# Kernel tuning notes

Measured on AMD Instinct MI355X. Metric: run time of the kernel, lower is better.

The kernel has to match this reference:

```python
import jax, jax.numpy as jnp
import numpy as np

N_NODES = 50000
BN_EPS = 1e-5


def graph_conv(x, row, col, ew, n):
    # deg from source indices only (matches torch.bincount(row))
    deg = jnp.zeros((n,), x.dtype).at[row].add(1.0)
    dinv = jnp.where(deg > 0, deg ** -0.5, 0.0)
    norm = dinv[row] * ew * dinv[col]                     # [E]
    msg = norm[:, None] * x[row]                          # [E, F]
    return jax.ops.segment_sum(msg, col, num_segments=n)  # out[dst] += w * x[src]


def batch_norm(x, gamma, beta):
    # training-mode BN over the node (batch) dim, biased variance
    mu = jnp.mean(x, axis=0)
    var = jnp.mean((x - mu) ** 2, axis=0)
    return (x - mu) / jnp.sqrt(var + BN_EPS) * gamma + beta


def setup_inputs() -> dict:
    key = jax.random.key(0)
    ks = jax.random.split(key, 12)
    node_features = jax.random.normal(ks[0], (N_NODES, 100), dtype=jnp.float32)
    edge_index = jax.random.randint(ks[1], (2, 800000), 0, N_NODES, dtype=jnp.int64)
    edge_weights = jax.random.uniform(ks[2], (800000,), dtype=jnp.float32)
    def lin(k, fi, fo):
        lim = 1.0 / np.sqrt(fi)
        k1, k2 = jax.random.split(k)
        W = jax.random.uniform(k1, (fi, fo), minval=-lim, maxval=lim, dtype=jnp.float32)
        b = jax.random.uniform(k2, (fo,), minval=-lim, maxval=lim, dtype=jnp.float32)
        return W, b
    W0, b0 = lin(ks[3], 100, 128)
    W1, b1 = lin(ks[4], 128, 128)
    W2, b2 = lin(ks[5], 128, 64)
    return {
        "node_features": node_features, "edge_index": edge_index, "edge_weights": edge_weights,
        "W0": W0, "b0": b0, "g0": jnp.ones((128,), jnp.float32), "be0": jnp.zeros((128,), jnp.float32),
        "W1": W1, "b1": b1, "g1": jnp.ones((128,), jnp.float32), "be1": jnp.zeros((128,), jnp.float32),
        "W2": W2, "b2": b2,
    }


def reference(node_features, edge_index, edge_weights,
              W0, b0, g0, be0, W1, b1, g1, be1, W2, b2):
    n = node_features.shape[0]
    row, col = edge_index[0], edge_index[1]
    x = node_features
    # layer 0
    x = graph_conv(x, row, col, edge_weights, n)
    x = jax.nn.relu(batch_norm(x @ W0 + b0, g0, be0))
    # layer 1
    x = graph_conv(x, row, col, edge_weights, n)
    x = jax.nn.relu(batch_norm(x @ W1 + b1, g1, be1))
    # final layer (no BN/relu)
    x = graph_conv(x, row, col, edge_weights, n)
    return x @ W2 + b2
```

## Files before the change

kernel.cpp:

```cpp
#include <hip/hip_runtime.h>
#include <cstdint>

#define F0 100
#define FH 128
#define FO 64
#define PD 4
#define BN_EPS 1e-5f

typedef unsigned short ushort_t;
typedef unsigned int uint_t;

static inline int ceil_div(long long a, long long b) { return (int)((a + b - 1) / b); }

__device__ __forceinline__ float bf_lo(uint_t w) { return __uint_as_float(w << 16); }
__device__ __forceinline__ float bf_hi(uint_t w) { return __uint_as_float(w & 0xffff0000u); }
__device__ __forceinline__ uint_t f2bf(float f) {
  uint_t u = __float_as_uint(f);
  return (u + 0x7fffu + ((u >> 16) & 1u)) >> 16;
}
__device__ __forceinline__ uint_t pack2(float a, float b) {
  return f2bf(a) | (f2bf(b) << 16);
}


template <int K, int F, int TM, int BK, bool BN_A, bool A_BF16, bool OUT_BF16>
__device__ __forceinline__ void gemm2_body(int bid, const void* __restrict__ A_,
                                           const float* __restrict__ W,
                                           const float* __restrict__ bias,
                                           const float* __restrict__ scA,
                                           const float* __restrict__ shA,
                                           void* __restrict__ out_, int n) {
  constexpr int NCG = F / 4;
  constexpr int NRG = 256 / NCG;
  constexpr int BR = NRG * TM;
  constexpr int F4 = F / 4;

  __shared__ float sW[BK][F];
  __shared__ float sA[BR][BK];

  const int tid = threadIdx.x;
  const int cg = tid % NCG;
  const int rg = tid / NCG;
  const int row0 = bid * BR;

  float4 acc[TM];
#pragma unroll
  for (int t = 0; t < TM; ++t) acc[t] = make_float4(0.f, 0.f, 0.f, 0.f);

  const float4* W4 = (const float4*)W;
  const float4 z4 = make_float4(0.f, 0.f, 0.f, 0.f);

  for (int k0 = 0; k0 < K; k0 += BK) {
    for (int i = tid; i < BK * F4; i += 256) {
      int kk = i / F4, f4 = i % F4;
      int gk = k0 + kk;
      ((float4*)&sW[kk][0])[f4] = (gk < K) ? W4[(size_t)gk * F4 + f4] : z4;
    }
    for (int i = tid; i < BR * (BK / 4); i += 256) {
      int r = i / (BK / 4), k4 = i % (BK / 4);
      int gr = row0 + r;
      int gk = k0 + k4 * 4;
      float4 av = z4;
      if (gr < n && gk + 3 < K) {
        if (A_BF16) {
          uint2 u = ((const uint2*)A_)[(size_t)gr * (K / 4) + (gk >> 2)];
          av.x = bf_lo(u.x); av.y = bf_hi(u.x);
          av.z = bf_lo(u.y); av.w = bf_hi(u.y);
        } else {
          av = ((const float4*)A_)[(size_t)gr * (K / 4) + (gk >> 2)];
        }
        if (BN_A) {
          float4 sc = ((const float4*)scA)[gk >> 2];
          float4 sh = ((const float4*)shA)[gk >> 2];
          av.x = fmaxf(fmaf(av.x, sc.x, sh.x), 0.f);
          av.y = fmaxf(fmaf(av.y, sc.y, sh.y), 0.f);
          av.z = fmaxf(fmaf(av.z, sc.z, sh.z), 0.f);
          av.w = fmaxf(fmaf(av.w, sc.w, sh.w), 0.f);
        }
      }
      ((float4*)&sA[r][0])[k4] = av;
    }
    __syncthreads();
#pragma unroll 4
    for (int kk = 0; kk < BK; ++kk) {
      float4 w = ((const float4*)&sW[kk][0])[cg];
#pragma unroll
      for (int t = 0; t < TM; ++t) {
        float a = sA[rg * TM + t][kk];
        acc[t].x = fmaf(a, w.x, acc[t].x);
        acc[t].y = fmaf(a, w.y, acc[t].y);
        acc[t].z = fmaf(a, w.z, acc[t].z);
        acc[t].w = fmaf(a, w.w, acc[t].w);
      }
    }
    __syncthreads();
  }

  float4 bb = bias ? ((const float4*)bias)[cg] : z4;
#pragma unroll
  for (int t = 0; t < TM; ++t) {
    int gr = row0 + rg * TM + t;
    if (gr < n) {
      float4 v = acc[t];
      v.x += bb.x; v.y += bb.y; v.z += bb.z; v.w += bb.w;
      if (OUT_BF16) {
        ((uint2*)out_)[(size_t)gr * F4 + cg] = make_uint2(pack2(v.x, v.y), pack2(v.z, v.w));
      } else {
        ((float4*)out_)[(size_t)gr * F4 + cg] = v;
      }
    }
  }
}

template <int K, int F, int TM, int BK, bool BN_A, bool A_BF16, bool OUT_BF16>
__global__ __launch_bounds__(256) void gemm2_kernel(const void* __restrict__ A,
                                                    const float* __restrict__ W,
                                                    const float* __restrict__ bias,
                                                    const float* __restrict__ scA,
                                                    const float* __restrict__ shA,
                                                    void* __restrict__ out, int n) {
  gemm2_body<K, F, TM, BK, BN_A, A_BF16, OUT_BF16>(blockIdx.x, A, W, bias, scA, shA, out, n);
}


__global__ __launch_bounds__(256) void fused_gemm_hist_kernel(
    const float* __restrict__ A, const float* __restrict__ W, void* __restrict__ out, int n,
    int GB, const int* __restrict__ row, const int* __restrict__ col,
    int* __restrict__ degr_p, int* __restrict__ degc_p, int* __restrict__ posw, int E) {
  int bid = blockIdx.x;
  int r5 = bid % 5;
  int g = bid / 5;
  if (r5 == 0 && g < GB) {
    gemm2_body<F0, FH, 8, 16, false, false, true>(g, A, W, nullptr, nullptr, nullptr, out, n);
    return;
  }
  int h = (r5 == 0) ? (bid - GB) : (bid - (g + 1));
  int e = h * 256 + threadIdx.x;
  if (e >= E) return;
  atomicAdd(&degr_p[(size_t)row[e] * PD], 1);
  posw[e] = atomicAdd(&degc_p[(size_t)col[e] * PD], 1);
}


__global__ __launch_bounds__(256) void scan_fused_kernel(const int* __restrict__ degr_p,
                                                         const int* __restrict__ degc_p,
                                                         float* __restrict__ dinv,
                                                         int* __restrict__ startp,
                                                         int* __restrict__ bsums, int n,
                                                         int* __restrict__ ctr) {
  __shared__ int s[256];
  const int tid = threadIdx.x;
  int i = blockIdx.x * 256 + tid;
  int dc = 0;
  if (i < n) {
    int dr = degr_p[(size_t)i * PD];
    dc = degc_p[(size_t)i * PD];
    dinv[i] = (dr > 0) ? rsqrtf((float)dr) : 0.0f;
  }
  s[tid] = dc;
  __syncthreads();
  for (int off = 1; off < 256; off <<= 1) {
    int t = 0;
    if (tid >= off) t = s[tid - off];
    __syncthreads();
    if (tid >= off) s[tid] += t;
    __syncthreads();
  }
  if (i < n) startp[i] = s[tid] - dc;
  if (tid == 255) bsums[blockIdx.x] = s[255];
  __threadfence();
  __syncthreads();
  __shared__ int lastFlag;
  if (tid == 0) lastFlag = (atomicAdd(ctr, 1) == (int)gridDim.x - 1) ? 1 : 0;
  __syncthreads();
  if (!lastFlag) return;
  int nb = (int)gridDim.x;
  int v = (tid < nb) ? atomicAdd(&bsums[tid], 0) : 0;
  s[tid] = v;
  __syncthreads();
  for (int off = 1; off < 256; off <<= 1) {
    int t = 0;
    if (tid >= off) t = s[tid - off];
    __syncthreads();
    if (tid >= off) s[tid] += t;
    __syncthreads();
  }
  if (tid < nb) bsums[tid] = s[tid] - v;
}


__global__ __launch_bounds__(256) void csr_scatter2_kernel(const int* __restrict__ row,
                                                           const int* __restrict__ col,
                                                           const float* __restrict__ ew,
                                                           const float* __restrict__ dinv,
                                                           const int* __restrict__ startp,
                                                           const int* __restrict__ bsums,
                                                           const int* __restrict__ posw,
                                                           int2* __restrict__ ep, int E) {
  int e = blockIdx.x * blockDim.x + threadIdx.x;
  if (e >= E) return;
  int r = row[e], c = col[e];
  int pos = startp[c] + bsums[c >> 8] + posw[e];
  float coef = dinv[r] * ew[e] * dinv[c];
  ep[pos] = make_int2(r, __float_as_int(coef));
}


template <int F, bool DO_BN, bool OUT_F32>
__global__ __launch_bounds__(256) void conv_kernel(const ushort_t* __restrict__ x,
                                                   const int* __restrict__ startp,
                                                   const int* __restrict__ bsums,
                                                   const int* __restrict__ degc_p,
                                                   const int2* __restrict__ ep,
                                                   const float* __restrict__ bias,
                                                   const float* __restrict__ scale,
                                                   const float* __restrict__ shift,
                                                   void* __restrict__ out, int n) {
  constexpr int G2 = F / 8;
  constexpr int TPD = G2 / 2;
  long long tid = (long long)blockIdx.x * 256 + threadIdx.x;
  if (tid >= (long long)n * TPD) return;
  int dst = (int)(tid / TPD);
  int q = (int)(tid % TPD);
  int s0 = startp[dst] + bsums[dst >> 8];
  int d = degc_p[(size_t)dst * PD];
  const uint4* x4 = (const uint4*)x;

  float sc[16], sh[16];
  if (DO_BN) {
#pragma unroll
    for (int ch = 0; ch < 2; ++ch) {
      int g = q + ch * TPD;
#pragma unroll
      for (int j = 0; j < 8; ++j) {
        sc[ch * 8 + j] = scale[g * 8 + j];
        sh[ch * 8 + j] = shift[g * 8 + j];
      }
    }
  }

  float acc[16];
#pragma unroll
  for (int j = 0; j < 16; ++j) acc[j] = 0.f;

  for (int k = 0; k < d; ++k) {
    int2 e = ep[s0 + k];
    float c = __int_as_float(e.y);
    const uint4* xp = x4 + (size_t)e.x * G2 + q;
    uint4 v0 = xp[0];
    uint4 v1 = xp[TPD];
    uint_t vv[8] = {v0.x, v0.y, v0.z, v0.w, v1.x, v1.y, v1.z, v1.w};
#pragma unroll
    for (int hh = 0; hh < 8; ++hh) {
      float f0 = bf_lo(vv[hh]);
      float f1 = bf_hi(vv[hh]);
      if (DO_BN) {
        f0 = fmaxf(fmaf(f0, sc[2 * hh], sh[2 * hh]), 0.f);
        f1 = fmaxf(fmaf(f1, sc[2 * hh + 1], sh[2 * hh + 1]), 0.f);
      }
      acc[2 * hh] = fmaf(c, f0, acc[2 * hh]);
      acc[2 * hh + 1] = fmaf(c, f1, acc[2 * hh + 1]);
    }
  }

  if (bias) {
#pragma unroll
    for (int ch = 0; ch < 2; ++ch) {
      int g = q + ch * TPD;
#pragma unroll
      for (int j = 0; j < 8; ++j) acc[ch * 8 + j] += bias[g * 8 + j];
    }
  }

  if (OUT_F32) {
    float4* o4 = (float4*)out;
    size_t base = (size_t)dst * (F / 4);
    o4[base + 2 * q] = make_float4(acc[0], acc[1], acc[2], acc[3]);
    o4[base + 2 * q + 1] = make_float4(acc[4], acc[5], acc[6], acc[7]);
    o4[base + 2 * (q + TPD)] = make_float4(acc[8], acc[9], acc[10], acc[11]);
    o4[base + 2 * (q + TPD) + 1] = make_float4(acc[12], acc[13], acc[14], acc[15]);
  } else {
    uint4* o4 = (uint4*)out;
    size_t base = (size_t)dst * G2;
    o4[base + q] = make_uint4(pack2(acc[0], acc[1]), pack2(acc[2], acc[3]),
                              pack2(acc[4], acc[5]), pack2(acc[6], acc[7]));
    o4[base + q + TPD] = make_uint4(pack2(acc[8], acc[9]), pack2(acc[10], acc[11]),
                                    pack2(acc[12], acc[13]), pack2(acc[14], acc[15]));
  }
}


__global__ __launch_bounds__(256) void bn_stats_fast_kernel(const ushort_t* __restrict__ z,
                                                            float* __restrict__ sum,
                                                            float* __restrict__ sumsq,
                                                            const float* __restrict__ g,
                                                            const float* __restrict__ be,
                                                            float* __restrict__ scale,
                                                            float* __restrict__ shift,
                                                            int n, int* __restrict__ ctr) {
  const int tid = threadIdx.x;
  const int q = tid & 15;
  const int rg = tid >> 4;
  const uint4* z4 = (const uint4*)z;

  float s[8], s2[8];
#pragma unroll
  for (int j = 0; j < 8; ++j) { s[j] = 0.f; s2[j] = 0.f; }

  for (int r = blockIdx.x * 16 + rg; r < n; r += (int)gridDim.x * 16) {
    uint4 v = z4[(size_t)r * (FH / 8) + q];
    uint_t vv[4] = {v.x, v.y, v.z, v.w};
#pragma unroll
    for (int h = 0; h < 4; ++h) {
      float f0 = bf_lo(vv[h]);
      float f1 = bf_hi(vv[h]);
      s[2 * h] += f0;      s2[2 * h] += f0 * f0;
      s[2 * h + 1] += f1;  s2[2 * h + 1] += f1 * f1;
    }
  }

  __shared__ float red[256][8];
#pragma unroll
  for (int j = 0; j < 8; ++j) red[tid][j] = s[j];
  __syncthreads();
  for (int off = 128; off >= 16; off >>= 1) {
    if (tid < off) {
#pragma unroll
      for (int j = 0; j < 8; ++j) red[tid][j] += red[tid + off][j];
    }
    __syncthreads();
  }
  if (tid < 16) {
#pragma unroll
    for (int j = 0; j < 8; ++j) unsafeAtomicAdd(&sum[8 * tid + j], red[tid][j]);
  }
  __syncthreads();
#pragma unroll
  for (int j = 0; j < 8; ++j) red[tid][j] = s2[j];
  __syncthreads();
  for (int off = 128; off >= 16; off >>= 1) {
    if (tid < off) {
#pragma unroll
      for (int j = 0; j < 8; ++j) red[tid][j] += red[tid + off][j];
    }
    __syncthreads();
  }
  if (tid < 16) {
#pragma unroll
    for (int j = 0; j < 8; ++j) unsafeAtomicAdd(&sumsq[8 * tid + j], red[tid][j]);
  }
  __threadfence();
  __syncthreads();
  __shared__ int lastFlag;
  if (tid == 0) lastFlag = (atomicAdd(ctr, 1) == (int)gridDim.x - 1) ? 1 : 0;
  __syncthreads();
  if (lastFlag && tid < FH) {
    float S = atomicAdd(&sum[tid], 0.0f);
    float S2 = atomicAdd(&sumsq[tid], 0.0f);
    float invN = 1.0f / (float)n;
    float mean = S * invN;
    float var = fmaxf(S2 * invN - mean * mean, 0.0f);
    float sc = g[tid] / sqrtf(var + BN_EPS);
    scale[tid] = sc;
    shift[tid] = be[tid] - mean * sc;
  }
}


extern "C" void kernel_launch(void* const* d_in, const int* in_sizes, int n_in,
                              void* d_out, int out_size, void* d_ws, size_t ws_size,
                              hipStream_t stream) {
  const float* x   = (const float*)d_in[0];
  const int*   ei  = (const int*)d_in[1];
  const float* ew  = (const float*)d_in[2];
  const float* W0  = (const float*)d_in[3];
  const float* b0  = (const float*)d_in[4];
  const float* g0  = (const float*)d_in[5];
  const float* be0 = (const float*)d_in[6];
  const float* W1  = (const float*)d_in[7];
  const float* b1  = (const float*)d_in[8];
  const float* g1  = (const float*)d_in[9];
  const float* be1 = (const float*)d_in[10];
  const float* W2  = (const float*)d_in[11];
  const float* b2  = (const float*)d_in[12];

  const int n = in_sizes[0] / F0;
  const int E = in_sizes[2];
  const int* row = ei;
  const int* col = ei + E;

  ushort_t* bufA  = (ushort_t*)d_ws;
  ushort_t* bufB  = bufA + (size_t)n * FH;
  int2*   ep      = (int2*)(bufB + (size_t)n * FH);
  int*    degc_p  = (int*)(ep + E);
  int*    degr_p  = degc_p + (size_t)n * PD;
  float*  sum0    = (float*)(degr_p + (size_t)n * PD);
  float*  sumsq0  = sum0 + FH;
  float*  sum1    = sumsq0 + FH;
  float*  sumsq1  = sum1 + FH;
  int*    ctr     = (int*)(sumsq1 + FH);
  const size_t zero_bytes = (2 * (size_t)n * PD + 4 * FH + 3) * 4;
  int*    startp  = ctr + 3;
  float*  dinv    = (float*)(startp + n);
  int*    bsums   = (int*)(dinv + n);
  float*  scale0  = (float*)(bsums + 256);
  float*  shift0  = scale0 + FH;
  float*  scale1  = shift0 + FH;
  float*  shift1  = scale1 + FH;
  int*    posw    = (int*)bufB;

  const int nb = ceil_div(n, 256);
  const int GB = ceil_div(n, 64);
  const int HB = ceil_div(E, 256);
  const int CB_H = ceil_div((long long)n * (FH / 16), 256);
  const int CB_O = ceil_div((long long)n * (FO / 16), 256);

  (void)hipMemsetAsync(degc_p, 0, zero_bytes, stream);
  fused_gemm_hist_kernel<<<GB + HB, 256, 0, stream>>>(x, W0, bufA, n, GB, row, col,
                                                      degr_p, degc_p, posw, E);
  scan_fused_kernel<<<nb, 256, 0, stream>>>(degr_p, degc_p, dinv, startp, bsums, n, ctr + 0);
  csr_scatter2_kernel<<<HB, 256, 0, stream>>>(row, col, ew, dinv, startp, bsums, posw, ep, E);
  conv_kernel<FH, false, false><<<CB_H, 256, 0, stream>>>(
      bufA, startp, bsums, degc_p, ep, b0, nullptr, nullptr, bufB, n);
  bn_stats_fast_kernel<<<128, 256, 0, stream>>>(bufB, sum0, sumsq0, g0, be0, scale0, shift0,
                                                n, ctr + 1);
  conv_kernel<FH, true, false><<<CB_H, 256, 0, stream>>>(
      bufB, startp, bsums, degc_p, ep, nullptr, scale0, shift0, bufA, n);
  gemm2_kernel<FH, FH, 8, 32, false, true, true><<<GB, 256, 0, stream>>>(
      bufA, W1, b1, nullptr, nullptr, bufB, n);
  bn_stats_fast_kernel<<<128, 256, 0, stream>>>(bufB, sum1, sumsq1, g1, be1, scale1, shift1,
                                                n, ctr + 2);
  gemm2_kernel<FH, FO, 4, 32, true, true, true><<<GB, 256, 0, stream>>>(
      bufB, W2, nullptr, scale1, shift1, bufA, n);
  conv_kernel<FO, false, true><<<CB_O, 256, 0, stream>>>(
      bufA, startp, bsums, degc_p, ep, b2, nullptr, nullptr, (float*)d_out, n);
}
```

Measured before the change: 367.4 us.

## Fuse BatchNorm statistics into conv0 and gemm1 epilogues, drop separate stats passes

Removes the two standalone BN statistics kernels. The per-feature sum and sum-of-squares are now accumulated in the epilogues of the first aggregation kernel and the W1 GEMM kernel, each followed by an in-block reduction, global atomics and a last-block finalize of scale and shift. This avoids re-reading the 50000x128 bf16 intermediates twice and saves two launches. In exchange, every block now issues atomics and runs an extra shared-memory reduction. Statistics are also taken from the fp32 values before bf16 rounding, which slightly changes the numerics.

```diff
diff --git a/kernel.cpp b/kernel.cpp
--- a/kernel.cpp
+++ b/kernel.cpp
@@ -206,6 +206,134 @@
 }
 
 
+template <bool DO_BN>
+__device__ __forceinline__ void conv_accum_128(const ushort_t* __restrict__ x, int s0, int d,
+                                               int q, const int2* __restrict__ ep,
+                                               const float* __restrict__ sc,
+                                               const float* __restrict__ sh,
+                                               float* __restrict__ acc) {
+  constexpr int G2 = FH / 8;
+  constexpr int TPD = 8;
+  const uint4* x4 = (const uint4*)x;
+#pragma unroll
+  for (int j = 0; j < 16; ++j) acc[j] = 0.f;
+  for (int k = 0; k < d; ++k) {
+    int2 e = ep[s0 + k];
+    float c = __int_as_float(e.y);
+    const uint4* xp = x4 + (size_t)e.x * G2 + q;
+    uint4 v0 = xp[0];
+    uint4 v1 = xp[TPD];
+    uint_t vv[8] = {v0.x, v0.y, v0.z, v0.w, v1.x, v1.y, v1.z, v1.w};
+#pragma unroll
+    for (int hh = 0; hh < 8; ++hh) {
+      float f0 = bf_lo(vv[hh]);
+      float f1 = bf_hi(vv[hh]);
+      if (DO_BN) {
+        f0 = fmaxf(fmaf(f0, sc[2 * hh], sh[2 * hh]), 0.f);
+        f1 = fmaxf(fmaf(f1, sc[2 * hh + 1], sh[2 * hh + 1]), 0.f);
+      }
+      acc[2 * hh] = fmaf(c, f0, acc[2 * hh]);
+      acc[2 * hh + 1] = fmaf(c, f1, acc[2 * hh + 1]);
+    }
+  }
+}
+
+
+__global__ __launch_bounds__(256) void conv0_stats_kernel(
+    const ushort_t* __restrict__ x, const int* __restrict__ startp,
+    const int* __restrict__ bsums, const int* __restrict__ degc_p,
+    const int2* __restrict__ ep, const float* __restrict__ bias,
+    ushort_t* __restrict__ out, int n, const float* __restrict__ g,
+    const float* __restrict__ be, float* __restrict__ sum, float* __restrict__ sumsq,
+    float* __restrict__ scale, float* __restrict__ shift, int* __restrict__ ctr) {
+  const int tid = threadIdx.x;
+  const int dl = tid / 8;
+  const int q = tid % 8;
+
+  float s[16], s2[16];
+#pragma unroll
+  for (int j = 0; j < 16; ++j) { s[j] = 0.f; s2[j] = 0.f; }
+
+  for (int c = 0; c < 2; ++c) {
+    int dst = blockIdx.x * 64 + c * 32 + dl;
+    if (dst >= n) continue;
+    int s0 = startp[dst] + bsums[dst >> 8];
+    int d = degc_p[(size_t)dst * PD];
+    float acc[16];
+    conv_accum_128<false>(x, s0, d, q, ep, nullptr, nullptr, acc);
+#pragma unroll
+    for (int ch = 0; ch < 2; ++ch) {
+#pragma unroll
+      for (int j = 0; j < 8; ++j) {
+        int f = ch * 64 + 8 * q + j;
+        float v = acc[ch * 8 + j] + bias[f];
+        acc[ch * 8 + j] = v;
+        s[ch * 8 + j] += v;
+        s2[ch * 8 + j] += v * v;
+      }
+    }
+    uint4* o4 = (uint4*)out;
+    size_t base = (size_t)dst * (FH / 8);
+    o4[base + q] = make_uint4(pack2(acc[0], acc[1]), pack2(acc[2], acc[3]),
+                              pack2(acc[4], acc[5]), pack2(acc[6], acc[7]));
+    o4[base + q + 8] = make_uint4(pack2(acc[8], acc[9]), pack2(acc[10], acc[11]),
+                                  pack2(acc[12], acc[13]), pack2(acc[14], acc[15]));
+  }
+
+  __shared__ float red[32][8][16];
+#pragma unroll
+  for (int j = 0; j < 16; ++j) red[dl][q][j] = s[j];
+  __syncthreads();
+  for (int off = 16; off >= 1; off >>= 1) {
+    if (dl < off) {
+#pragma unroll
+      for (int j = 0; j < 16; ++j) red[dl][q][j] += red[dl + off][q][j];
+    }
+    __syncthreads();
+  }
+  if (dl == 0) {
+#pragma unroll
+    for (int j = 0; j < 16; ++j) {
+      int f = (j < 8) ? (8 * q + j) : (64 + 8 * q + (j - 8));
+      unsafeAtomicAdd(&sum[f], red[0][q][j]);
+    }
+  }
+  __syncthreads();
+#pragma unroll
+  for (int j = 0; j < 16; ++j) red[dl][q][j] = s2[j];
+  __syncthreads();
+  for (int off = 16; off >= 1; off >>= 1) {
+    if (dl < off) {
+#pragma unroll
+      for (int j = 0; j < 16; ++j) red[dl][q][j] += red[dl + off][q][j];
+    }
+    __syncthreads();
+  }
+  if (dl == 0) {
+#pragma unroll
+    for (int j = 0; j < 16; ++j) {
+      int f = (j < 8) ? (8 * q + j) : (64 + 8 * q + (j - 8));
+      unsafeAtomicAdd(&sumsq[f], red[0][q][j]);
+    }
+  }
+  __threadfence();
+  __syncthreads();
+  __shared__ int lastFlag;
+  if (tid == 0) lastFlag = (atomicAdd(ctr, 1) == (int)gridDim.x - 1) ? 1 : 0;
+  __syncthreads();
+  if (lastFlag && tid < FH) {
+    float S = atomicAdd(&sum[tid], 0.0f);
+    float S2 = atomicAdd(&sumsq[tid], 0.0f);
+    float invN = 1.0f / (float)n;
+    float mean = S * invN;
+    float var = fmaxf(S2 * invN - mean * mean, 0.0f);
+    float sc = g[tid] / sqrtf(var + BN_EPS);
+    scale[tid] = sc;
+    shift[tid] = be[tid] - mean * sc;
+  }
+}
+
+
 template <int F, bool DO_BN, bool OUT_F32>
 __global__ __launch_bounds__(256) void conv_kernel(const ushort_t* __restrict__ x,
                                                    const int* __restrict__ startp,
@@ -290,64 +418,107 @@
 }
 
 
-__global__ __launch_bounds__(256) void bn_stats_fast_kernel(const ushort_t* __restrict__ z,
-                                                            float* __restrict__ sum,
-                                                            float* __restrict__ sumsq,
-                                                            const float* __restrict__ g,
-                                                            const float* __restrict__ be,
-                                                            float* __restrict__ scale,
-                                                            float* __restrict__ shift,
-                                                            int n, int* __restrict__ ctr) {
+__global__ __launch_bounds__(256) void gemm1_stats_kernel(
+    const ushort_t* __restrict__ A, const float* __restrict__ W,
+    const float* __restrict__ bias, ushort_t* __restrict__ out, int n,
+    const float* __restrict__ g, const float* __restrict__ be, float* __restrict__ sum,
+    float* __restrict__ sumsq, float* __restrict__ scale, float* __restrict__ shift,
+    int* __restrict__ ctr) {
+  constexpr int K = FH, F = FH, TM = 8, BK = 32;
+  constexpr int NCG = F / 4;
+  constexpr int NRG = 256 / NCG;
+  constexpr int BR = NRG * TM;
+  constexpr int F4 = F / 4;
+
+  __shared__ float sW[BK][F];
+  __shared__ float sA[BR][BK];
+  __shared__ float red[NRG][NCG][4];
+
   const int tid = threadIdx.x;
-  const int q = tid & 15;
-  const int rg = tid >> 4;
-  const uint4* z4 = (const uint4*)z;
-
-  float s[8], s2[8];
-#pragma unroll
-  for (int j = 0; j < 8; ++j) { s[j] = 0.f; s2[j] = 0.f; }
-
-  for (int r = blockIdx.x * 16 + rg; r < n; r += (int)gridDim.x * 16) {
-    uint4 v = z4[(size_t)r * (FH / 8) + q];
-    uint_t vv[4] = {v.x, v.y, v.z, v.w};
-#pragma unroll
-    for (int h = 0; h < 4; ++h) {
-      float f0 = bf_lo(vv[h]);
-      float f1 = bf_hi(vv[h]);
-      s[2 * h] += f0;      s2[2 * h] += f0 * f0;
-      s[2 * h + 1] += f1;  s2[2 * h + 1] += f1 * f1;
-    }
-  }
-
-  __shared__ float red[256][8];
-#pragma unroll
-  for (int j = 0; j < 8; ++j) red[tid][j] = s[j];
-  __syncthreads();
-  for (int off = 128; off >= 16; off >>= 1) {
-    if (tid < off) {
-#pragma unroll
-      for (int j = 0; j < 8; ++j) red[tid][j] += red[tid + off][j];
-    }
-    __syncthreads();
-  }
-  if (tid < 16) {
-#pragma unroll
-    for (int j = 0; j < 8; ++j) unsafeAtomicAdd(&sum[8 * tid + j], red[tid][j]);
-  }
-  __syncthreads();
-#pragma unroll
-  for (int j = 0; j < 8; ++j) red[tid][j] = s2[j];
-  __syncthreads();
-  for (int off = 128; off >= 16; off >>= 1) {
-    if (tid < off) {
-#pragma unroll
-      for (int j = 0; j < 8; ++j) red[tid][j] += red[tid + off][j];
-    }
-    __syncthreads();
-  }
-  if (tid < 16) {
-#pragma unroll
-    for (int j = 0; j < 8; ++j) unsafeAtomicAdd(&sumsq[8 * tid + j], red[tid][j]);
+  const int cg = tid % NCG;
+  const int rg = tid / NCG;
+  const int row0 = blockIdx.x * BR;
+
+  float4 acc[TM];
+#pragma unroll
+  for (int t = 0; t < TM; ++t) acc[t] = make_float4(0.f, 0.f, 0.f, 0.f);
+
+  const float4* W4 = (const float4*)W;
+  const float4 z4 = make_float4(0.f, 0.f, 0.f, 0.f);
+
+  for (int k0 = 0; k0 < K; k0 += BK) {
+    for (int i = tid; i < BK * F4; i += 256) {
+      int kk = i / F4, f4 = i % F4;
+      ((float4*)&sW[kk][0])[f4] = W4[(size_t)(k0 + kk) * F4 + f4];
+    }
+    for (int i = tid; i < BR * (BK / 4); i += 256) {
+      int r = i / (BK / 4), k4 = i % (BK / 4);
+      int gr = row0 + r;
+      int gk = k0 + k4 * 4;
+      float4 av = z4;
+      if (gr < n) {
+        uint2 u = ((const uint2*)A)[(size_t)gr * (K / 4) + (gk >> 2)];
+        av.x = bf_lo(u.x); av.y = bf_hi(u.x);
+        av.z = bf_lo(u.y); av.w = bf_hi(u.y);
+      }
+      ((float4*)&sA[r][0])[k4] = av;
+    }
+    __syncthreads();
+#pragma unroll 4
+    for (int kk = 0; kk < BK; ++kk) {
+      float4 w = ((const float4*)&sW[kk][0])[cg];
+#pragma unroll
+      for (int t = 0; t < TM; ++t) {
+        float a = sA[rg * TM + t][kk];
+        acc[t].x = fmaf(a, w.x, acc[t].x);
+        acc[t].y = fmaf(a, w.y, acc[t].y);
+        acc[t].z = fmaf(a, w.z, acc[t].z);
+        acc[t].w = fmaf(a, w.w, acc[t].w);
+      }
+    }
+    __syncthreads();
+  }
+
+  float4 bb = ((const float4*)bias)[cg];
+  float4 s = z4, s2 = z4;
+#pragma unroll
+  for (int t = 0; t < TM; ++t) {
+    int gr = row0 + rg * TM + t;
+    if (gr < n) {
+      float4 v = acc[t];
+      v.x += bb.x; v.y += bb.y; v.z += bb.z; v.w += bb.w;
+      ((uint2*)out)[(size_t)gr * F4 + cg] = make_uint2(pack2(v.x, v.y), pack2(v.z, v.w));
+      s.x += v.x; s.y += v.y; s.z += v.z; s.w += v.w;
+      s2.x += v.x * v.x; s2.y += v.y * v.y; s2.z += v.z * v.z; s2.w += v.w * v.w;
+    }
+  }
+
+  red[rg][cg][0] = s.x; red[rg][cg][1] = s.y; red[rg][cg][2] = s.z; red[rg][cg][3] = s.w;
+  __syncthreads();
+  for (int off = 4; off >= 1; off >>= 1) {
+    if (rg < off) {
+#pragma unroll
+      for (int j = 0; j < 4; ++j) red[rg][cg][j] += red[rg + off][cg][j];
+    }
+    __syncthreads();
+  }
+  if (rg == 0) {
+#pragma unroll
+    for (int j = 0; j < 4; ++j) unsafeAtomicAdd(&sum[cg * 4 + j], red[0][cg][j]);
+  }
+  __syncthreads();
+  red[rg][cg][0] = s2.x; red[rg][cg][1] = s2.y; red[rg][cg][2] = s2.z; red[rg][cg][3] = s2.w;
+  __syncthreads();
+  for (int off = 4; off >= 1; off >>= 1) {
+    if (rg < off) {
+#pragma unroll
+      for (int j = 0; j < 4; ++j) red[rg][cg][j] += red[rg + off][cg][j];
+    }
+    __syncthreads();
+  }
+  if (rg == 0) {
+#pragma unroll
+    for (int j = 0; j < 4; ++j) unsafeAtomicAdd(&sumsq[cg * 4 + j], red[0][cg][j]);
   }
   __threadfence();
   __syncthreads();
@@ -412,6 +583,7 @@
   const int nb = ceil_div(n, 256);
   const int GB = ceil_div(n, 64);
   const int HB = ceil_div(E, 256);
+  const int CB0 = ceil_div(n, 64);
   const int CB_H = ceil_div((long long)n * (FH / 16), 256);
   const int CB_O = ceil_div((long long)n * (FO / 16), 256);
 
@@ -420,16 +592,12 @@
                                                       degr_p, degc_p, posw, E);
   scan_fused_kernel<<<nb, 256, 0, stream>>>(degr_p, degc_p, dinv, startp, bsums, n, ctr + 0);
   csr_scatter2_kernel<<<HB, 256, 0, stream>>>(row, col, ew, dinv, startp, bsums, posw, ep, E);
-  conv_kernel<FH, false, false><<<CB_H, 256, 0, stream>>>(
-      bufA, startp, bsums, degc_p, ep, b0, nullptr, nullptr, bufB, n);
-  bn_stats_fast_kernel<<<128, 256, 0, stream>>>(bufB, sum0, sumsq0, g0, be0, scale0, shift0,
-                                                n, ctr + 1);
+  conv0_stats_kernel<<<CB0, 256, 0, stream>>>(bufA, startp, bsums, degc_p, ep, b0, bufB, n,
+                                              g0, be0, sum0, sumsq0, scale0, shift0, ctr + 1);
   conv_kernel<FH, true, false><<<CB_H, 256, 0, stream>>>(
       bufB, startp, bsums, degc_p, ep, nullptr, scale0, shift0, bufA, n);
-  gemm2_kernel<FH, FH, 8, 32, false, true, true><<<GB, 256, 0, stream>>>(
-      bufA, W1, b1, nullptr, nullptr, bufB, n);
-  bn_stats_fast_kernel<<<128, 256, 0, stream>>>(bufB, sum1, sumsq1, g1, be1, scale1, shift1,
-                                                n, ctr + 2);
+  gemm1_stats_kernel<<<GB, 256, 0, stream>>>(bufA, W1, b1, bufB, n, g1, be1, sum1, sumsq1,
+                                             scale1, shift1, ctr + 2);
   gemm2_kernel<FH, FO, 4, 32, true, true, true><<<GB, 256, 0, stream>>>(
       bufB, W2, nullptr, scale1, shift1, bufA, n);
   conv_kernel<FO, false, true><<<CB_O, 256, 0, stream>>>(
```

Measured after the change: 576.9 us. 57.0% more time.

## Replace scalar FMA GEMMs for layers 1 and 2 with bf16 MFMA kernel

Applied to the files above, without the earlier changes.

Adds a GEMM kernel built on the 16x16x32 bf16 MFMA instruction, with weights converted to bf16 and packed into shared memory in fragment order. It replaces the scalar tiled GEMMs for the W1 and W2 projections and folds the BN-plus-ReLU on the input into the A-fragment load. The aim is to move the dense matmul work onto matrix cores instead of vector FMAs. In exchange, weights are rounded to bf16, which may change numerics, and the output is stored as scattered 2-byte writes.

```diff
diff --git a/kernel.cpp b/kernel.cpp
--- a/kernel.cpp
+++ b/kernel.cpp
@@ -9,6 +9,8 @@
 
 typedef unsigned short ushort_t;
 typedef unsigned int uint_t;
+typedef __attribute__((ext_vector_type(8))) __bf16 bf16x8;
+typedef __attribute__((ext_vector_type(4))) float f32x4;
 
 static inline int ceil_div(long long a, long long b) { return (int)((a + b - 1) / b); }
 
@@ -112,14 +114,84 @@
   }
 }
 
-template <int K, int F, int TM, int BK, bool BN_A, bool A_BF16, bool OUT_BF16>
-__global__ __launch_bounds__(256) void gemm2_kernel(const void* __restrict__ A,
-                                                    const float* __restrict__ W,
-                                                    const float* __restrict__ bias,
-                                                    const float* __restrict__ scA,
-                                                    const float* __restrict__ shA,
-                                                    void* __restrict__ out, int n) {
-  gemm2_body<K, F, TM, BK, BN_A, A_BF16, OUT_BF16>(blockIdx.x, A, W, bias, scA, shA, out, n);
+
+template <int FOUT, bool BN_A>
+__global__ __launch_bounds__(256) void gemm_mfma_kernel(const ushort_t* __restrict__ A,
+                                                        const float* __restrict__ W,
+                                                        const float* __restrict__ bias,
+                                                        const float* __restrict__ scA,
+                                                        const float* __restrict__ shA,
+                                                        ushort_t* __restrict__ out, int n) {
+  constexpr int F4 = FOUT / 4;
+  constexpr int NT = FOUT / 16;
+  __shared__ ushort_t Wt[16 * FOUT * 8];
+
+  const int tid = threadIdx.x;
+  const float4* W4 = (const float4*)W;
+  uint_t* w32 = (uint_t*)Wt;
+  for (int idx = tid; idx < 64 * F4; idx += 256) {
+    int kp = idx / F4, cq = idx % F4;
+    float4 wa = W4[(size_t)(2 * kp) * F4 + cq];
+    float4 wb = W4[(size_t)(2 * kp + 1) * F4 + cq];
+    int kq = kp >> 2, e2 = kp & 3;
+    int base = (kq * FOUT + cq * 4) * 4 + e2;
+    w32[base]      = pack2(wa.x, wb.x);
+    w32[base + 4]  = pack2(wa.y, wb.y);
+    w32[base + 8]  = pack2(wa.z, wb.z);
+    w32[base + 12] = pack2(wa.w, wb.w);
+  }
+  __syncthreads();
+
+  const int l = tid & 63;
+  const int wv = tid >> 6;
+  const int cc = l & 15;
+  const int h = l >> 4;
+  const int rowa = blockIdx.x * 64 + wv * 16 + cc;
+  const int ra = (rowa < n) ? rowa : (n - 1);
+
+  f32x4 acc[NT];
+#pragma unroll
+  for (int t = 0; t < NT; ++t) acc[t] = (f32x4)0.f;
+
+#pragma unroll
+  for (int ks = 0; ks < 4; ++ks) {
+    const int k0 = 32 * ks;
+    uint4 av = *(const uint4*)(A + (size_t)ra * FH + k0 + 8 * h);
+    if (BN_A) {
+      const float4* sc4 = (const float4*)(scA + k0 + 8 * h);
+      const float4* sh4 = (const float4*)(shA + k0 + 8 * h);
+      float4 sa = sc4[0], sb = sc4[1], ha = sh4[0], hb = sh4[1];
+      av.x = pack2(fmaxf(fmaf(bf_lo(av.x), sa.x, ha.x), 0.f),
+                   fmaxf(fmaf(bf_hi(av.x), sa.y, ha.y), 0.f));
+      av.y = pack2(fmaxf(fmaf(bf_lo(av.y), sa.z, ha.z), 0.f),
+                   fmaxf(fmaf(bf_hi(av.y), sa.w, ha.w), 0.f));
+      av.z = pack2(fmaxf(fmaf(bf_lo(av.z), sb.x, hb.x), 0.f),
+                   fmaxf(fmaf(bf_hi(av.z), sb.y, hb.y), 0.f));
+      av.w = pack2(fmaxf(fmaf(bf_lo(av.w), sb.z, hb.z), 0.f),
+                   fmaxf(fmaf(bf_hi(av.w), sb.w, hb.w), 0.f));
+    }
+    bf16x8 afrag = __builtin_bit_cast(bf16x8, av);
+    const int kq = ks * 4 + h;
+#pragma unroll
+    for (int ct = 0; ct < NT; ++ct) {
+      int c = ct * 16 + cc;
+      uint4 bv = *(const uint4*)(Wt + ((size_t)kq * FOUT + c) * 8);
+      bf16x8 bfrag = __builtin_bit_cast(bf16x8, bv);
+      acc[ct] = __builtin_amdgcn_mfma_f32_16x16x32_bf16(afrag, bfrag, acc[ct], 0, 0, 0);
+    }
+  }
+
+  const int rbase = blockIdx.x * 64 + wv * 16 + 4 * h;
+#pragma unroll
+  for (int ct = 0; ct < NT; ++ct) {
+    int c = ct * 16 + cc;
+    float bvv = bias ? bias[c] : 0.f;
+#pragma unroll
+    for (int r = 0; r < 4; ++r) {
+      int gr = rbase + r;
+      if (gr < n) out[(size_t)gr * FOUT + c] = (ushort_t)f2bf(acc[ct][r] + bvv);
+    }
+  }
 }
 
 
@@ -412,6 +484,7 @@
   const int nb = ceil_div(n, 256);
   const int GB = ceil_div(n, 64);
   const int HB = ceil_div(E, 256);
+  const int MB = ceil_div(n, 64);
   const int CB_H = ceil_div((long long)n * (FH / 16), 256);
   const int CB_O = ceil_div((long long)n * (FO / 16), 256);
 
@@ -426,12 +499,10 @@
                                                 n, ctr + 1);
   conv_kernel<FH, true, false><<<CB_H, 256, 0, stream>>>(
       bufB, startp, bsums, degc_p, ep, nullptr, scale0, shift0, bufA, n);
-  gemm2_kernel<FH, FH, 8, 32, false, true, true><<<GB, 256, 0, stream>>>(
-      bufA, W1, b1, nullptr, nullptr, bufB, n);
+  gemm_mfma_kernel<FH, false><<<MB, 256, 0, stream>>>(bufA, W1, b1, nullptr, nullptr, bufB, n);
   bn_stats_fast_kernel<<<128, 256, 0, stream>>>(bufB, sum1, sumsq1, g1, be1, scale1, shift1,
                                                 n, ctr + 2);
-  gemm2_kernel<FH, FO, 4, 32, true, true, true><<<GB, 256, 0, stream>>>(
-      bufB, W2, nullptr, scale1, shift1, bufA, n);
+  gemm_mfma_kernel<FO, true><<<MB, 256, 0, stream>>>(bufB, W2, nullptr, scale1, shift1, bufA, n);
   conv_kernel<FO, false, true><<<CB_O, 256, 0, stream>>>(
       bufA, startp, bsums, degc_p, ep, b2, nullptr, nullptr, (float*)d_out, n);
 }
```

Measured after the change: 342.6 us. -6.8%, faster.
